# Kernel optimization log

Measured on AMD Instinct MI355X. Metric: run time of the kernel, lower is better.

The kernel has to match this reference:

```python
import jax, jax.numpy as jnp
import numpy as np

EPS = 1e-5
K_NUM, EDGE_TYPE = 5, 2  # k_num = A_fixed_partitions(3) + edge_type(2)


def _bn(x, gamma, beta):
    # training-mode BatchNorm2d: batch stats over (N, T, V) per channel
    m = jnp.mean(x, axis=(0, 2, 3), keepdims=True)
    v = jnp.var(x, axis=(0, 2, 3), keepdims=True)
    return (x - m) * jax.lax.rsqrt(v + EPS) * gamma[None, :, None, None] + beta[None, :, None, None]


def setup_inputs() -> dict:
    key = jax.random.key(0)
    ks = jax.random.split(key, 6)
    N, C, T, V = 32, 64, 300, 25
    Cout, Kt = 64, 9
    x = jax.random.normal(ks[0], (N, C, T, V), jnp.float32)
    A = jax.random.uniform(ks[1], (K_NUM - EDGE_TYPE, V, V), jnp.float32) / V  # fixed adjacency (already scaled by edge_importance)
    B = jax.random.uniform(ks[2], (N, EDGE_TYPE, V, V), jnp.float32) / V      # per-sample adaptive adjacency A_act
    lamda_act = jnp.full((1,), 0.5, jnp.float32)
    conv_w = jax.random.normal(ks[3], (Cout * K_NUM, C), jnp.float32) * (1.0 / np.sqrt(C))  # 1x1 conv weight
    conv_b = jnp.zeros((Cout * K_NUM,), jnp.float32)
    bn1_g = jnp.ones((Cout,), jnp.float32)
    bn1_b = jnp.zeros((Cout,), jnp.float32)
    tcn_w = jax.random.normal(ks[4], (Cout, Cout, Kt, 1), jnp.float32) * (1.0 / np.sqrt(Cout * Kt))
    tcn_b = jnp.zeros((Cout,), jnp.float32)
    bn2_g = jnp.ones((Cout,), jnp.float32)
    bn2_b = jnp.zeros((Cout,), jnp.float32)
    return dict(x=x, A=A, B=B, lamda_act=lamda_act, conv_w=conv_w, conv_b=conv_b,
                bn1_g=bn1_g, bn1_b=bn1_b, tcn_w=tcn_w, tcn_b=tcn_b, bn2_g=bn2_g, bn2_b=bn2_b)


def reference(x, A, B, lamda_act, conv_w, conv_b, bn1_g, bn1_b, tcn_w, tcn_b, bn2_g, bn2_b):
    n, c, t, v = x.shape
    res = x  # identity residual (in_ch == out_ch, stride 1)
    # SpatialGcn: 1x1 conv (pure channel GEMM) -> split -> dual einsum graph conv
    y = jnp.einsum('nctv,oc->notv', x, conv_w) + conv_b[None, :, None, None]  # (n, K*Cout, t, v)
    cout = y.shape[1] // K_NUM
    y = y.reshape(n, K_NUM, cout, t, v)
    x1 = jnp.einsum('nkctv,kvw->nctw', y[:, :K_NUM - EDGE_TYPE], A)   # fixed adjacency
    x2 = jnp.einsum('nkctv,nkvw->nctw', y[:, K_NUM - EDGE_TYPE:], B)  # adaptive adjacency
    g = x1 + x2 * lamda_act[0]
    # tcn: BN -> ReLU -> temporal conv (9,1) pad (4,0) -> BN -> Dropout(0)=identity
    h = jax.nn.relu(_bn(g, bn1_g, bn1_b))
    h = jax.lax.conv_general_dilated(h, tcn_w, window_strides=(1, 1),
                                     padding=((4, 4), (0, 0)),
                                     dimension_numbers=('NCHW', 'OIHW', 'NCHW'))
    h = h + tcn_b[None, :, None, None]
    h = _bn(h, bn2_g, bn2_b)
    return jax.nn.relu(h + res)
```

## Files before the change

### kernel.cpp

```cpp
#include <hip/hip_runtime.h>
#include <hip/hip_bf16.h>

#define N_  32
#define C_  64
#define T_  300
#define V_  25
#define TV  (T_*V_)
#define CTV (C_*TV)
#define NELEM (N_*CTV)
#define CNTF 240000.0f
#define PROWS 7788

typedef float f32x4 __attribute__((ext_vector_type(4)));
typedef short bf16x8 __attribute__((ext_vector_type(8)));
typedef short s4v __attribute__((ext_vector_type(4)));
typedef short s8v __attribute__((ext_vector_type(8)));

__device__ __forceinline__ unsigned short f2bf(float f) {
    unsigned u = __float_as_uint(f);
    unsigned r = u + 0x7fffu + ((u >> 16) & 1u);
    return (unsigned short)(r >> 16);
}
__device__ __forceinline__ float bf2f(unsigned short u) {
    return __uint_as_float(((unsigned)u) << 16);
}
__device__ __forceinline__ unsigned cvt_pk(float lo, float hi) {
    unsigned r;
    asm("v_cvt_pk_bf16_f32 %0, %1, %2" : "=v"(r) : "v"(lo), "v"(hi));
    return r;
}

__global__ __launch_bounds__(256) void k_prep(
    const float* __restrict__ conv_w, const float* __restrict__ tw,
    unsigned short* __restrict__ w2b, unsigned short* __restrict__ twb)
{
    int tid = blockIdx.x*256 + threadIdx.x;
    for (int e = tid; e < 20480; e += 8192) {
        int ks = e >> 11, c = (e >> 5) & 63, kk = e & 31;
        w2b[e] = f2bf(conv_w[(((ks>>1)*64 + c)*64) + (ks&1)*32 + kk]);
    }
    for (int e = tid; e < 36864; e += 8192) {
        int gi = e >> 11, c = (e >> 5) & 63, kk = e & 31;
        int dt = gi >> 1, ks = gi & 1;
        twb[e] = f2bf(tw[(c*64 + 32*ks + kk)*9 + dt]);
    }
}

__global__ __launch_bounds__(256) void k_gcn(
    const float* __restrict__ x, const float* __restrict__ A,
    const float* __restrict__ B, const float* __restrict__ lamda,
    const unsigned short* __restrict__ w2b, const float* __restrict__ conv_b,
    unsigned short* __restrict__ gout, float* __restrict__ stats3)
{
    __shared__ unsigned short ash[5*32*40];
    __shared__ unsigned short zsh[32*328];
    __shared__ float csum[160];
    __shared__ float sbc[320];

    const int tb = blockIdx.x, n = blockIdx.y;
    const int t0 = tb*10;
    const int tid = threadIdx.x;
    const int lane = tid & 63, wv = tid >> 6;
    const int lg = lane >> 4, lr = lane & 15;
    const int crow = lr + 16*wv;
    const int cbase = 16*wv + 4*lg;

    bf16x8 wfrag[10];
    #pragma unroll
    for (int ks = 0; ks < 10; ++ks)
        wfrag[ks] = *(const bf16x8*)&w2b[(ks*64 + crow)*32 + 8*lg];

    const float lam = lamda[0];
    {
        s8v z8 = {0,0,0,0,0,0,0,0};
        for (int e = tid; e < 800; e += 256) *(s8v*)&ash[e*8] = z8;
    }
    for (int e = tid; e < 320; e += 256) sbc[e] = conv_b[e];
    __syncthreads();
    for (int e = tid; e < 3125; e += 256) {
        int k = e / 625, r = e - k*625;
        int v = r / 25, w = r - v*25;
        float val = (k < 3) ? A[e] : lam * B[((n<<1) + (k-3))*625 + r];
        ash[k*1280 + w*40 + v] = f2bf(val);
    }
    __syncthreads();
    for (int e = tid; e < 160; e += 256) {
        int k = e / 32, w = e % 32;
        float s = 0.f;
        for (int v = 0; v < 25; ++v) s += bf2f(ash[k*1280 + w*40 + v]);
        csum[e] = s;
    }
    __syncthreads();

    float bs0[4], bs1[4];
    #pragma unroll
    for (int r = 0; r < 4; ++r) {
        float s0 = 0.f, s1 = 0.f;
        #pragma unroll
        for (int k = 0; k < 5; ++k) {
            float cb = sbc[k*64 + cbase + r];
            s0 += cb * csum[k*32 + lr];
            s1 += cb * csum[k*32 + lr + 16];
        }
        bs0[r] = s0; bs1[r] = s1;
    }

    float sacc[4] = {0,0,0,0}, qacc[4] = {0,0,0,0};

    const float* xrow = x + n*CTV + crow*TV + t0*V_;
    float xf[8];
    #pragma unroll
    for (int i = 0; i < 8; ++i) { int v = 8*lg + i; xf[i] = (v < 25) ? xrow[v] : 0.f; }

    for (int tl = 0; tl < 10; ++tl) {
        union { bf16x8 v; unsigned u[4]; } xu;
        #pragma unroll
        for (int p = 0; p < 4; ++p) xu.u[p] = cvt_pk(xf[2*p], xf[2*p+1]);
        bf16x8 xfrag = xu.v;
        if (tl < 9) {
            const float* xn = xrow + (tl+1)*V_;
            #pragma unroll
            for (int i = 0; i < 8; ++i) { int v = 8*lg + i; xf[i] = (v < 25) ? xn[v] : 0.f; }
        }
        #pragma unroll
        for (int k = 0; k < 5; ++k)
        #pragma unroll
        for (int nt = 0; nt < 2; ++nt) {
            bf16x8 bfrag = *(const bf16x8*)&ash[k*1280 + (lr + 16*nt)*40 + 8*lg];
            f32x4 z = {0.f,0.f,0.f,0.f};
            z = __builtin_amdgcn_mfma_f32_16x16x32_bf16(xfrag, bfrag, z, 0, 0, 0);
            uint2 zz;
            zz.x = cvt_pk(z[0], z[1]);
            zz.y = cvt_pk(z[2], z[3]);
            *(uint2*)&zsh[(lr + 16*nt)*328 + k*64 + 16*wv + 4*lg] = zz;
        }
        __syncthreads();
        f32x4 acc0 = {0.f,0.f,0.f,0.f}, acc1 = {0.f,0.f,0.f,0.f};
        #pragma unroll
        for (int ks = 0; ks < 10; ++ks) {
            bf16x8 b0 = *(const bf16x8*)&zsh[lr*328 + 32*ks + 8*lg];
            bf16x8 b1 = *(const bf16x8*)&zsh[(lr+16)*328 + 32*ks + 8*lg];
            acc0 = __builtin_amdgcn_mfma_f32_16x16x32_bf16(wfrag[ks], b0, acc0, 0, 0, 0);
            acc1 = __builtin_amdgcn_mfma_f32_16x16x32_bf16(wfrag[ks], b1, acc1, 0, 0, 0);
        }
        float v0a[4], v1a[4];
        #pragma unroll
        for (int r = 0; r < 4; ++r) {
            v0a[r] = acc0[r] + bs0[r];
            v1a[r] = acc1[r] + bs1[r];
            sacc[r] += v0a[r] + (lr < 9 ? v1a[r] : 0.f);
            qacc[r] += v0a[r]*v0a[r] + (lr < 9 ? v1a[r]*v1a[r] : 0.f);
        }
        unsigned short* grow = gout + (size_t)(n*300 + t0 + tl)*1600;
        uint2 g0, g1;
        g0.x = cvt_pk(v0a[0], v0a[1]); g0.y = cvt_pk(v0a[2], v0a[3]);
        g1.x = cvt_pk(v1a[0], v1a[1]); g1.y = cvt_pk(v1a[2], v1a[3]);
        *(uint2*)&grow[lr*64 + cbase] = g0;
        if (lr < 9) *(uint2*)&grow[(lr+16)*64 + cbase] = g1;
        __syncthreads();
    }

    #pragma unroll
    for (int r = 0; r < 4; ++r) {
        float s = sacc[r], q = qacc[r];
        s += __shfl_xor(s, 1); s += __shfl_xor(s, 2);
        s += __shfl_xor(s, 4); s += __shfl_xor(s, 8);
        q += __shfl_xor(q, 1); q += __shfl_xor(q, 2);
        q += __shfl_xor(q, 4); q += __shfl_xor(q, 8);
        if (lr == 0) {
            stats3[(n*30 + tb)*128 + cbase + r] = s;
            stats3[(n*30 + tb)*128 + 64 + cbase + r] = q;
        }
    }
}

__global__ __launch_bounds__(256) void k_fin(
    const float* __restrict__ src, int count, float* __restrict__ sbo,
    const float* __restrict__ gma, const float* __restrict__ bta)
{
    const int c = blockIdx.x, tid = threadIdx.x;
    float s = 0.f, q = 0.f;
    for (int b = tid; b < count; b += 256) {
        s += src[b*128 + c];
        q += src[b*128 + 64 + c];
    }
    #pragma unroll
    for (int m = 1; m < 64; m <<= 1) { s += __shfl_xor(s, m); q += __shfl_xor(q, m); }
    __shared__ float rs[4], rq[4];
    if ((tid & 63) == 0) { rs[tid>>6] = s; rq[tid>>6] = q; }
    __syncthreads();
    if (tid == 0) {
        s = rs[0]+rs[1]+rs[2]+rs[3]; q = rq[0]+rq[1]+rq[2]+rq[3];
        float mean = s / CNTF, var = q / CNTF - mean*mean;
        float sc = gma[c] * rsqrtf(var + 1e-5f);
        sbo[c] = sc;
        sbo[64 + c] = bta[c] - mean*sc;
    }
}

__global__ __launch_bounds__(256) void k_bn1(
    const unsigned short* __restrict__ g, const float* __restrict__ sb,
    unsigned short* __restrict__ p)
{
    __shared__ float sbs[128];
    if (threadIdx.x < 128) sbs[threadIdx.x] = sb[threadIdx.x];
    __syncthreads();
    int idx = blockIdx.x*256 + threadIdx.x;
    int n = idx / (PROWS*8);
    int rem = idx - n*(PROWS*8);
    int row = (rem >> 3) - 128;
    int q8 = (rem & 7) * 8;
    uint4 out4 = {0,0,0,0};
    if (row >= 0 && row < 7500) {
        s8v raw = *(const s8v*)&g[((size_t)n*7500 + row)*64 + q8];
        float f[8];
        #pragma unroll
        for (int j = 0; j < 8; ++j)
            f[j] = fmaxf(fmaf(bf2f((unsigned short)raw[j]), sbs[q8+j], sbs[64+q8+j]), 0.f);
        out4.x = cvt_pk(f[0], f[1]); out4.y = cvt_pk(f[2], f[3]);
        out4.z = cvt_pk(f[4], f[5]); out4.w = cvt_pk(f[6], f[7]);
    }
    *(uint4*)&p[(size_t)idx*8] = out4;
}

__global__ __launch_bounds__(256) void k_tcn(
    const unsigned short* __restrict__ p, const unsigned short* __restrict__ twb,
    const float* __restrict__ tb, unsigned short* __restrict__ hout,
    float* __restrict__ stats4)
{
    __shared__ unsigned short lds[328*64];

    const int bj = blockIdx.x, n = blockIdx.y;
    const int j0 = bj*128;
    const int tid = threadIdx.x;
    const int lane = tid & 63, ct = tid >> 6;
    const int lg = lane >> 4, lr = lane & 15;
    const int cA = ct*16 + lr;
    const int cbase = ct*16 + 4*lg;

    const unsigned short* psrc = p + ((size_t)n*PROWS + 28 + j0)*64;
    for (int e = tid; e < 2624; e += 256) {
        int row = e >> 3, q = e & 7;
        s8v v = *(const s8v*)&psrc[(size_t)row*64 + q*8];
        *(s8v*)&lds[row*64 + ((q ^ (row & 7)))*8] = v;
    }

    f32x4 acc[8];
    #pragma unroll
    for (int i = 0; i < 8; ++i) acc[i] = (f32x4){0.f,0.f,0.f,0.f};
    float tbc[4];
    #pragma unroll
    for (int r = 0; r < 4; ++r) tbc[r] = tb[cbase + r];

    __syncthreads();

    #pragma unroll
    for (int ks = 0; ks < 2; ++ks) {
        bf16x8 af[9];
        #pragma unroll
        for (int dt = 0; dt < 9; ++dt)
            af[dt] = *(const bf16x8*)&twb[((2*dt + ks)*64 + cA)*32 + 8*lg];
        #pragma unroll
        for (int jt = 0; jt < 8; ++jt) {
            #pragma unroll
            for (int dt = 0; dt < 9; ++dt) {
                int row = 16*jt + lr + 25*dt;
                bf16x8 b = *(const bf16x8*)&lds[row*64 + ((4*ks + lg) ^ (row & 7))*8];
                acc[jt] = __builtin_amdgcn_mfma_f32_16x16x32_bf16(af[dt], b, acc[jt], 0, 0, 0);
            }
        }
    }

    float sacc[4] = {0,0,0,0}, qacc[4] = {0,0,0,0};
    #pragma unroll
    for (int jt = 0; jt < 8; ++jt) {
        int j = j0 + 16*jt + lr;
        if (j < 7500) {
            #pragma unroll
            for (int r = 0; r < 4; ++r) {
                float v = acc[jt][r] + tbc[r];
                sacc[r] += v; qacc[r] += v*v;
            }
        }
    }
    #pragma unroll
    for (int r = 0; r < 4; ++r) {
        float s = sacc[r], q = qacc[r];
        s += __shfl_xor(s, 1); s += __shfl_xor(s, 2);
        s += __shfl_xor(s, 4); s += __shfl_xor(s, 8);
        q += __shfl_xor(q, 1); q += __shfl_xor(q, 2);
        q += __shfl_xor(q, 4); q += __shfl_xor(q, 8);
        if (lr == 0) {
            float* dst = stats4 + (size_t)(n*59 + bj)*128;
            dst[cbase + r] = s;
            dst[64 + cbase + r] = q;
        }
    }

    __syncthreads();
    #pragma unroll
    for (int jt = 0; jt < 8; ++jt)
        #pragma unroll
        for (int r = 0; r < 4; ++r)
            lds[(cbase + r)*136 + 16*jt + lr] = f2bf(acc[jt][r] + tbc[r]);
    __syncthreads();
    for (int e = tid; e < 2048; e += 256) {
        int row = e >> 5, c4 = (e & 31) << 2;
        int j = j0 + c4;
        if (j < 7500)
            *(s4v*)&hout[(size_t)(n*64 + row)*7500 + j] = *(const s4v*)&lds[row*136 + c4];
    }
}

__global__ __launch_bounds__(256) void k_out(
    const unsigned short* __restrict__ h, const float* __restrict__ x,
    const float* __restrict__ sb, float* __restrict__ out)
{
    int i4 = blockIdx.x * 256 + threadIdx.x;
    if (i4 >= NELEM/4) return;
    int c = ((i4*4) / TV) & 63;
    float s2 = sb[128 + c], b2 = sb[192 + c];
    s4v hv = *(const s4v*)&h[i4*4];
    float4 xv = ((const float4*)x)[i4];
    float4 o;
    o.x = fmaxf(fmaf(bf2f((unsigned short)hv[0]), s2, b2) + xv.x, 0.f);
    o.y = fmaxf(fmaf(bf2f((unsigned short)hv[1]), s2, b2) + xv.y, 0.f);
    o.z = fmaxf(fmaf(bf2f((unsigned short)hv[2]), s2, b2) + xv.z, 0.f);
    o.w = fmaxf(fmaf(bf2f((unsigned short)hv[3]), s2, b2) + xv.w, 0.f);
    ((float4*)out)[i4] = o;
}

extern "C" void kernel_launch(void* const* d_in, const int* in_sizes, int n_in,
                              void* d_out, int out_size, void* d_ws, size_t ws_size,
                              hipStream_t stream)
{
    const float* x      = (const float*)d_in[0];
    const float* A      = (const float*)d_in[1];
    const float* B      = (const float*)d_in[2];
    const float* lamda  = (const float*)d_in[3];
    const float* conv_w = (const float*)d_in[4];
    const float* conv_b = (const float*)d_in[5];
    const float* bn1_g  = (const float*)d_in[6];
    const float* bn1_b  = (const float*)d_in[7];
    const float* tcn_w  = (const float*)d_in[8];
    const float* tcn_b  = (const float*)d_in[9];
    const float* bn2_g  = (const float*)d_in[10];
    const float* bn2_b  = (const float*)d_in[11];

    unsigned short* g = (unsigned short*)d_ws;
    unsigned short* p = g + NELEM;
    unsigned short* h = p + (size_t)N_*PROWS*64;
    float* stats3 = (float*)(h + NELEM);
    float* stats4 = stats3 + 960*128;
    float* sb     = stats4 + 1888*128;
    unsigned short* w2b = (unsigned short*)(sb + 256);
    unsigned short* twb = w2b + 20480;

    k_prep<<<32, 256, 0, stream>>>(conv_w, tcn_w, w2b, twb);
    k_gcn<<<dim3(30, N_), 256, 0, stream>>>(x, A, B, lamda, w2b, conv_b, g, stats3);
    k_fin<<<64, 256, 0, stream>>>(stats3, 960, sb, bn1_g, bn1_b);
    k_bn1<<<PROWS, 256, 0, stream>>>(g, sb, p);
    k_tcn<<<dim3(59, N_), 256, 0, stream>>>(p, twb, tcn_b, h, stats4);
    k_fin<<<64, 256, 0, stream>>>(stats4, 1888, sb + 128, bn2_g, bn2_b);
    k_out<<<NELEM/4/256, 256, 0, stream>>>(h, x, sb, (float*)d_out);
}
```

Baseline: 134.6 us.

## Precompute adjacency tiles in prep kernels and double gcn grid parallelism

Moves the per-block bf16 conversion and transposition of A and lambda*B, plus the column sums, into separate prep kernels. k_gcn now only copies the prepared tiles into shared memory. k_gcn also processes 5 time steps per block instead of 10, doubling the grid to 60x32 blocks and the number of BN1 partial-stat rows. This removes redundant setup work repeated in every block and improves occupancy, at the cost of an extra kernel launch and more partial stats for k_fin to reduce.

```diff
diff --git a/kernel.cpp b/kernel.cpp
--- a/kernel.cpp
+++ b/kernel.cpp
@@ -32,7 +32,9 @@
 
 __global__ __launch_bounds__(256) void k_prep(
     const float* __restrict__ conv_w, const float* __restrict__ tw,
-    unsigned short* __restrict__ w2b, unsigned short* __restrict__ twb)
+    const float* __restrict__ A,
+    unsigned short* __restrict__ w2b, unsigned short* __restrict__ twb,
+    unsigned short* __restrict__ ashA)
 {
     int tid = blockIdx.x*256 + threadIdx.x;
     for (int e = tid; e < 20480; e += 8192) {
@@ -44,21 +46,53 @@
         int dt = gi >> 1, ks = gi & 1;
         twb[e] = f2bf(tw[(c*64 + 32*ks + kk)*9 + dt]);
     }
+    for (int e = tid; e < 3840; e += 8192) {
+        int k = e / 1280, r = e - k*1280, w = r / 40, v = r % 40;
+        float val = (w < 25 && v < 25) ? A[k*625 + v*25 + w] : 0.f;
+        ashA[e] = f2bf(val);
+    }
+}
+
+__global__ __launch_bounds__(256) void k_prepn(
+    const float* __restrict__ A, const float* __restrict__ B,
+    const float* __restrict__ lamda,
+    unsigned short* __restrict__ bshB, float* __restrict__ csumN)
+{
+    const int n = blockIdx.x, tid = threadIdx.x;
+    const float lam = lamda[0];
+    unsigned short* dst = bshB + n*2560;
+    {
+        s8v z8 = {0,0,0,0,0,0,0,0};
+        for (int e = tid; e < 320; e += 256) *(s8v*)&dst[e*8] = z8;
+    }
+    __syncthreads();
+    for (int e = tid; e < 1250; e += 256) {
+        int k = e / 625, r = e - k*625, v = r / 25, w = r - v*25;
+        dst[k*1280 + w*40 + v] = f2bf(lam * B[((n<<1) + k)*625 + r]);
+    }
+    for (int e = tid; e < 160; e += 256) {
+        int k = e / 32, w = e % 32;
+        float s = 0.f;
+        if (w < 25) {
+            if (k < 3) { for (int v = 0; v < 25; ++v) s += bf2f(f2bf(A[k*625 + v*25 + w])); }
+            else       { for (int v = 0; v < 25; ++v) s += bf2f(f2bf(lam * B[((n<<1)+(k-3))*625 + v*25 + w])); }
+        }
+        csumN[n*160 + e] = s;
+    }
 }
 
 __global__ __launch_bounds__(256) void k_gcn(
-    const float* __restrict__ x, const float* __restrict__ A,
-    const float* __restrict__ B, const float* __restrict__ lamda,
+    const float* __restrict__ x,
+    const unsigned short* __restrict__ ashA, const unsigned short* __restrict__ bshB,
+    const float* __restrict__ csumN,
     const unsigned short* __restrict__ w2b, const float* __restrict__ conv_b,
     unsigned short* __restrict__ gout, float* __restrict__ stats3)
 {
-    __shared__ unsigned short ash[5*32*40];
-    __shared__ unsigned short zsh[32*328];
-    __shared__ float csum[160];
-    __shared__ float sbc[320];
+    __shared__ unsigned short ash[6400];
+    __shared__ unsigned short zsh[10496];
 
     const int tb = blockIdx.x, n = blockIdx.y;
-    const int t0 = tb*10;
+    const int t0 = tb*5;
     const int tid = threadIdx.x;
     const int lane = tid & 63, wv = tid >> 6;
     const int lg = lane >> 4, lr = lane & 15;
@@ -70,35 +104,19 @@
     for (int ks = 0; ks < 10; ++ks)
         wfrag[ks] = *(const bf16x8*)&w2b[(ks*64 + crow)*32 + 8*lg];
 
-    const float lam = lamda[0];
-    {
-        s8v z8 = {0,0,0,0,0,0,0,0};
-        for (int e = tid; e < 800; e += 256) *(s8v*)&ash[e*8] = z8;
-    }
-    for (int e = tid; e < 320; e += 256) sbc[e] = conv_b[e];
-    __syncthreads();
-    for (int e = tid; e < 3125; e += 256) {
-        int k = e / 625, r = e - k*625;
-        int v = r / 25, w = r - v*25;
-        float val = (k < 3) ? A[e] : lam * B[((n<<1) + (k-3))*625 + r];
-        ash[k*1280 + w*40 + v] = f2bf(val);
-    }
-    __syncthreads();
-    for (int e = tid; e < 160; e += 256) {
-        int k = e / 32, w = e % 32;
-        float s = 0.f;
-        for (int v = 0; v < 25; ++v) s += bf2f(ash[k*1280 + w*40 + v]);
-        csum[e] = s;
-    }
-    __syncthreads();
-
+    for (int e = tid; e < 480; e += 256)
+        *(s8v*)&ash[e*8] = *(const s8v*)&ashA[e*8];
+    for (int e = tid; e < 320; e += 256)
+        *(s8v*)&ash[3840 + e*8] = *(const s8v*)&bshB[n*2560 + e*8];
+
+    const float* csum = csumN + n*160;
     float bs0[4], bs1[4];
     #pragma unroll
     for (int r = 0; r < 4; ++r) {
         float s0 = 0.f, s1 = 0.f;
         #pragma unroll
         for (int k = 0; k < 5; ++k) {
-            float cb = sbc[k*64 + cbase + r];
+            float cb = conv_b[k*64 + cbase + r];
             s0 += cb * csum[k*32 + lr];
             s1 += cb * csum[k*32 + lr + 16];
         }
@@ -112,12 +130,14 @@
     #pragma unroll
     for (int i = 0; i < 8; ++i) { int v = 8*lg + i; xf[i] = (v < 25) ? xrow[v] : 0.f; }
 
-    for (int tl = 0; tl < 10; ++tl) {
+    __syncthreads();
+
+    for (int tl = 0; tl < 5; ++tl) {
         union { bf16x8 v; unsigned u[4]; } xu;
         #pragma unroll
         for (int p = 0; p < 4; ++p) xu.u[p] = cvt_pk(xf[2*p], xf[2*p+1]);
         bf16x8 xfrag = xu.v;
-        if (tl < 9) {
+        if (tl < 4) {
             const float* xn = xrow + (tl+1)*V_;
             #pragma unroll
             for (int i = 0; i < 8; ++i) { int v = 8*lg + i; xf[i] = (v < 25) ? xn[v] : 0.f; }
@@ -168,8 +188,8 @@
         q += __shfl_xor(q, 1); q += __shfl_xor(q, 2);
         q += __shfl_xor(q, 4); q += __shfl_xor(q, 8);
         if (lr == 0) {
-            stats3[(n*30 + tb)*128 + cbase + r] = s;
-            stats3[(n*30 + tb)*128 + 64 + cbase + r] = q;
+            stats3[(n*60 + tb)*128 + cbase + r] = s;
+            stats3[(n*60 + tb)*128 + 64 + cbase + r] = q;
         }
     }
 }
@@ -351,14 +371,18 @@
     unsigned short* p = g + NELEM;
     unsigned short* h = p + (size_t)N_*PROWS*64;
     float* stats3 = (float*)(h + NELEM);
-    float* stats4 = stats3 + 960*128;
+    float* stats4 = stats3 + 1920*128;
     float* sb     = stats4 + 1888*128;
-    unsigned short* w2b = (unsigned short*)(sb + 256);
-    unsigned short* twb = w2b + 20480;
-
-    k_prep<<<32, 256, 0, stream>>>(conv_w, tcn_w, w2b, twb);
-    k_gcn<<<dim3(30, N_), 256, 0, stream>>>(x, A, B, lamda, w2b, conv_b, g, stats3);
-    k_fin<<<64, 256, 0, stream>>>(stats3, 960, sb, bn1_g, bn1_b);
+    float* csumN  = sb + 256;
+    unsigned short* w2b  = (unsigned short*)(csumN + 32*160);
+    unsigned short* twb  = w2b + 20480;
+    unsigned short* ashA = twb + 36864;
+    unsigned short* bshB = ashA + 3840;
+
+    k_prep<<<32, 256, 0, stream>>>(conv_w, tcn_w, A, w2b, twb, ashA);
+    k_prepn<<<32, 256, 0, stream>>>(A, B, lamda, bshB, csumN);
+    k_gcn<<<dim3(60, N_), 256, 0, stream>>>(x, ashA, bshB, csumN, w2b, conv_b, g, stats3);
+    k_fin<<<64, 256, 0, stream>>>(stats3, 1920, sb, bn1_g, bn1_b);
     k_bn1<<<PROWS, 256, 0, stream>>>(g, sb, p);
     k_tcn<<<dim3(59, N_), 256, 0, stream>>>(p, twb, tcn_b, h, stats4);
     k_fin<<<64, 256, 0, stream>>>(stats4, 1888, sb + 128, bn2_g, bn2_b);
```

Result: slower. 139.7 us (+3.8%).
